# Performance work log

Measured on AMD Instinct MI355X. Metric: run time of the kernel, lower is better.

The kernel has to match this reference:

```python
import jax, jax.numpy as jnp
import numpy as np
import math

D_MODEL = 1024
N_HEADS = 16
D_K = D_MODEL // N_HEADS
MAX_REL = 128


def setup_inputs() -> dict:
    key = jax.random.key(0)
    ks = jax.random.split(key, 10)
    B, S = 2, 2048
    std = 1.0 / math.sqrt(D_MODEL)
    inp = {
        "x": jax.random.normal(ks[0], (B, S, D_MODEL), dtype=jnp.float32),
        "Wq": jax.random.normal(ks[1], (D_MODEL, D_MODEL), dtype=jnp.float32) * std,
        "bq": jnp.zeros((D_MODEL,), dtype=jnp.float32),
        "Wk": jax.random.normal(ks[2], (D_MODEL, D_MODEL), dtype=jnp.float32) * std,
        "bk": jnp.zeros((D_MODEL,), dtype=jnp.float32),
        "Wv": jax.random.normal(ks[3], (D_MODEL, D_MODEL), dtype=jnp.float32) * std,
        "bv": jnp.zeros((D_MODEL,), dtype=jnp.float32),
        "Wo": jax.random.normal(ks[4], (D_MODEL, D_MODEL), dtype=jnp.float32) * std,
        "bo": jnp.zeros((D_MODEL,), dtype=jnp.float32),
        "rel_bias": jax.random.normal(ks[5], (N_HEADS, 2 * MAX_REL + 1), dtype=jnp.float32) * 0.02,
    }
    return inp


def _rel_bias_matrix(rel_bias, seq_len):
    # (H, S, S) gathered relative-position bias
    pos = jnp.arange(seq_len)
    rel = pos[:, None] - pos[None, :]
    idx = jnp.clip(rel, -MAX_REL, MAX_REL) + MAX_REL  # (S, S) in [0, 2M]
    return rel_bias[:, idx]  # (H, S, S)


def reference(x, Wq, bq, Wk, bk, Wv, bv, Wo, bo, rel_bias):
    B, S, _ = x.shape
    def proj(W, b):
        y = x @ W.T + b  # torch Linear: x @ W^T + b
        return y.reshape(B, S, N_HEADS, D_K).transpose(0, 2, 1, 3)  # (B,H,S,Dk)
    Q, K, V = proj(Wq, bq), proj(Wk, bk), proj(Wv, bv)
    scores = jnp.einsum("bhqd,bhkd->bhqk", Q, K) / math.sqrt(D_K)
    scores = scores + _rel_bias_matrix(rel_bias, S)[None]
    attn = jax.nn.softmax(scores, axis=-1)
    out = jnp.einsum("bhqk,bhkd->bhqd", attn, V)
    out = out.transpose(0, 2, 1, 3).reshape(B, S, D_MODEL)
    return out @ Wo.T + bo
```

## Files before the change

### kernel.cpp

```cpp
#include <hip/hip_runtime.h>

static constexpr int DM = 1024;
static constexpr int NH = 16;
static constexpr int DK = 64;
static constexpr int S  = 2048;
static constexpr int B  = 2;
static constexpr float LOG2E = 1.4426950408889634f;
static constexpr float FMAX  = 11.0f;
static constexpr int NSPLIT = 4;

typedef _Float16 f16;
typedef _Float16 f16x8 __attribute__((ext_vector_type(8)));
typedef _Float16 f16x4 __attribute__((ext_vector_type(4)));
typedef float    f32x4 __attribute__((ext_vector_type(4)));

static constexpr size_t NX = (size_t)B * S * DM;
static constexpr size_t NW = (size_t)DM * DM;

__global__ __launch_bounds__(256) void cvt_f16(const float* __restrict__ x,
                                               const float* __restrict__ wq,
                                               const float* __restrict__ wk,
                                               const float* __restrict__ wv,
                                               const float* __restrict__ wo,
                                               f16* __restrict__ xh,
                                               f16* __restrict__ wqh,
                                               f16* __restrict__ wkh,
                                               f16* __restrict__ wvh,
                                               f16* __restrict__ woh)
{
    const size_t base = ((size_t)blockIdx.x * 256 + threadIdx.x) * 8;
    const float* src; f16* dst; size_t off;
    if (base < NX) { src = x; dst = xh; off = base; }
    else {
        const size_t rem = base - NX;
        const int seg = (int)(rem >> 20);
        off = rem & (NW - 1);
        src = seg == 0 ? wq : (seg == 1 ? wk : (seg == 2 ? wv : wo));
        dst = seg == 0 ? wqh : (seg == 1 ? wkh : (seg == 2 ? wvh : woh));
    }
    float4 a = *(const float4*)&src[off];
    float4 b = *(const float4*)&src[off + 4];
    f16x8 h = { (f16)a.x, (f16)a.y, (f16)a.z, (f16)a.w,
                (f16)b.x, (f16)b.y, (f16)b.z, (f16)b.w };
    *(f16x8*)&dst[off] = h;
}

template<int MODE>
__global__ __launch_bounds__(256) void gemm_h(const f16* __restrict__ A,
                                              const f16* __restrict__ W0,
                                              const f16* __restrict__ W1,
                                              const f16* __restrict__ W2,
                                              const float* __restrict__ b0,
                                              const float* __restrict__ b1,
                                              const float* __restrict__ b2,
                                              void* __restrict__ o0,
                                              void* __restrict__ o1,
                                              void* __restrict__ o2)
{
    __shared__ f16 As[128 * 72];
    __shared__ f16 Bs[128 * 72];

    const int t    = threadIdx.x;
    const int w    = t >> 6;
    const int lane = t & 63;
    const int tx   = lane & 15;
    const int quad = lane >> 4;
    const int wm   = w >> 1;
    const int wn   = w & 1;
    const int m0   = blockIdx.y * 128;

    const f16* W; const float* bias; f16* outh = nullptr; float* outf = nullptr;
    float scale; int n0;
    if (MODE == 0) {
        const int wsel = blockIdx.x >> 3;
        n0   = (blockIdx.x & 7) * 128;
        W    = wsel == 0 ? W0 : (wsel == 1 ? W1 : W2);
        bias = wsel == 0 ? b0 : (wsel == 1 ? b1 : b2);
        outh = (f16*)(wsel == 0 ? o0 : (wsel == 1 ? o1 : o2));
        scale = wsel == 0 ? LOG2E * 0.125f : 1.0f;
    } else {
        n0 = blockIdx.x * 128;
        W = W0; bias = b0; outf = (float*)o0; scale = 1.0f;
    }

    const int lr = t >> 2;
    const int lc = (t & 3) * 8;

    f32x4 acc[4][4];
#pragma unroll
    for (int mt = 0; mt < 4; ++mt)
#pragma unroll
        for (int nt = 0; nt < 4; ++nt) acc[mt][nt] = (f32x4){0.f, 0.f, 0.f, 0.f};

    f16x8 ga[4], gb[4];
    {
        const f16* Ap = A + (size_t)(m0 + lr) * DM + lc;
        const f16* Wp = W + (size_t)(n0 + lr) * DM + lc;
        ga[0] = *(const f16x8*)(Ap);
        ga[1] = *(const f16x8*)(Ap + 32);
        ga[2] = *(const f16x8*)(Ap + (size_t)64 * DM);
        ga[3] = *(const f16x8*)(Ap + (size_t)64 * DM + 32);
        gb[0] = *(const f16x8*)(Wp);
        gb[1] = *(const f16x8*)(Wp + 32);
        gb[2] = *(const f16x8*)(Wp + (size_t)64 * DM);
        gb[3] = *(const f16x8*)(Wp + (size_t)64 * DM + 32);
    }

    for (int k0 = 0; k0 < DM; k0 += 64) {
        __syncthreads();
        *(f16x8*)&As[ lr       * 72 + lc     ] = ga[0];
        *(f16x8*)&As[ lr       * 72 + lc + 32] = ga[1];
        *(f16x8*)&As[(lr + 64) * 72 + lc     ] = ga[2];
        *(f16x8*)&As[(lr + 64) * 72 + lc + 32] = ga[3];
        *(f16x8*)&Bs[ lr       * 72 + lc     ] = gb[0];
        *(f16x8*)&Bs[ lr       * 72 + lc + 32] = gb[1];
        *(f16x8*)&Bs[(lr + 64) * 72 + lc     ] = gb[2];
        *(f16x8*)&Bs[(lr + 64) * 72 + lc + 32] = gb[3];
        if (k0 + 64 < DM) {
            const f16* Ap = A + (size_t)(m0 + lr) * DM + k0 + 64 + lc;
            const f16* Wp = W + (size_t)(n0 + lr) * DM + k0 + 64 + lc;
            ga[0] = *(const f16x8*)(Ap);
            ga[1] = *(const f16x8*)(Ap + 32);
            ga[2] = *(const f16x8*)(Ap + (size_t)64 * DM);
            ga[3] = *(const f16x8*)(Ap + (size_t)64 * DM + 32);
            gb[0] = *(const f16x8*)(Wp);
            gb[1] = *(const f16x8*)(Wp + 32);
            gb[2] = *(const f16x8*)(Wp + (size_t)64 * DM);
            gb[3] = *(const f16x8*)(Wp + (size_t)64 * DM + 32);
        }
        __syncthreads();

        f16x8 af[4][2];
#pragma unroll
        for (int mt = 0; mt < 4; ++mt)
#pragma unroll
            for (int ks = 0; ks < 2; ++ks)
                af[mt][ks] = *(const f16x8*)&As[(wm*64 + mt*16 + tx)*72 + ks*32 + quad*8];
#pragma unroll
        for (int nt = 0; nt < 4; ++nt) {
#pragma unroll
            for (int ks = 0; ks < 2; ++ks) {
                f16x8 bf = *(const f16x8*)&Bs[(wn*64 + nt*16 + tx)*72 + ks*32 + quad*8];
#pragma unroll
                for (int mt = 0; mt < 4; ++mt)
                    acc[mt][nt] = __builtin_amdgcn_mfma_f32_16x16x32_f16(af[mt][ks], bf, acc[mt][nt], 0, 0, 0);
            }
        }
    }

#pragma unroll
    for (int nt = 0; nt < 4; ++nt) {
        const int n = n0 + wn*64 + nt*16 + tx;
        const float bn = bias[n];
#pragma unroll
        for (int mt = 0; mt < 4; ++mt)
#pragma unroll
            for (int r = 0; r < 4; ++r) {
                const int m = m0 + wm*64 + mt*16 + quad*4 + r;
                const float v = (acc[mt][nt][r] + bn) * scale;
                if (MODE == 0) {
                    const int bi = m >> 11;
                    const int ss = m & (S - 1);
                    const int h  = n >> 6;
                    const int dk = n & (DK - 1);
                    outh[((size_t)((bi*NH + h)*S + ss))*DK + dk] = (f16)v;
                } else {
                    outf[(size_t)m * DM + n] = v;
                }
            }
    }
}

__global__ __launch_bounds__(256, 4) void attn_v4(const f16* __restrict__ Q,
                                                  const f16* __restrict__ K,
                                                  const f16* __restrict__ V,
                                                  const float* __restrict__ relb,
                                                  f16* __restrict__ On,
                                                  float* __restrict__ lp)
{
    __shared__ f16 Ks[64*72];
    __shared__ f16 Vt[64*72];
    __shared__ float rb2[257];

    const int t    = threadIdx.x;
    const int w    = t >> 6;
    const int lane = t & 63;
    const int tx   = lane & 15;
    const int quad = lane >> 4;
    const int qt   = blockIdx.x >> 2;
    const int sp   = blockIdx.x & 3;
    const int h    = blockIdx.y;
    const int b    = blockIdx.z;
    const int q0   = qt * 128;

    const f16* Qb = Q + (size_t)((b*NH + h) * S) * DK;
    const f16* Kb = K + (size_t)((b*NH + h) * S) * DK;
    const f16* Vb = V + (size_t)((b*NH + h) * S) * DK;

    for (int i = t; i < 257; i += 256) rb2[i] = relb[h*257 + i] * LOG2E - FMAX;

    const int qrow = q0 + w*32 + tx;
    f16x8 qf[2][2];
#pragma unroll
    for (int qb = 0; qb < 2; ++qb)
#pragma unroll
        for (int ks = 0; ks < 2; ++ks)
            qf[qb][ks] = *(const f16x8*)(Qb + (size_t)(qrow + qb*16)*DK + ks*32 + quad*8);

    f32x4 oT[4][2];
    float lsum[2] = {0.f, 0.f};
#pragma unroll
    for (int d = 0; d < 4; ++d)
#pragma unroll
        for (int qb = 0; qb < 2; ++qb) oT[d][qb] = (f32x4){0.f, 0.f, 0.f, 0.f};

    const int kt0 = sp * (S / 64 / NSPLIT);
    for (int kt = kt0; kt < kt0 + S/64/NSPLIT; ++kt) {
        const int k0 = kt * 64;

        const int seq = t & 63, d0k = (t >> 6) * 16;
        f16x8 kr0 = *(const f16x8*)(Kb + (size_t)(k0 + seq)*DK + d0k);
        f16x8 kr1 = *(const f16x8*)(Kb + (size_t)(k0 + seq)*DK + d0k + 8);
        const int s2 = (t & 31) * 2, d0v = (t >> 5) * 8;
        f16x8 vr0 = *(const f16x8*)(Vb + (size_t)(k0 + s2    )*DK + d0v);
        f16x8 vr1 = *(const f16x8*)(Vb + (size_t)(k0 + s2 + 1)*DK + d0v);

        __syncthreads();
        *(f16x8*)&Ks[seq*72 + d0k    ] = kr0;
        *(f16x8*)&Ks[seq*72 + d0k + 8] = kr1;
        {
            const int g = ((s2 >> 2) & 3)*16 + (s2 >> 4)*4 + (s2 & 3);
            const unsigned short* u0 = (const unsigned short*)&vr0;
            const unsigned short* u1 = (const unsigned short*)&vr1;
#pragma unroll
            for (int j = 0; j < 8; ++j) {
                unsigned int pw = (unsigned int)u0[j] | ((unsigned int)u1[j] << 16);
                *(unsigned int*)&Vt[(d0v + j)*72 + g] = pw;
            }
        }
        __syncthreads();

        const bool farlo = (k0 - q0) >= 256;
        const bool farhi = (q0 - k0) >= 192;
        const float bconst = farlo ? rb2[0] : rb2[256];
        const int relbase = (q0 + w*32 + tx) - (k0 + quad*4);

        f16x4 pf[4][2];
#pragma unroll
        for (int sb = 0; sb < 4; ++sb) {
            f32x4 sT[2];
            if (farlo | farhi) {
                sT[0] = (f32x4){bconst, bconst, bconst, bconst};
                sT[1] = sT[0];
            } else {
#pragma unroll
                for (int qb = 0; qb < 2; ++qb)
#pragma unroll
                    for (int r = 0; r < 4; ++r) {
                        int rel = relbase + qb*16 - sb*16 - r;
                        rel = rel < -128 ? -128 : (rel > 128 ? 128 : rel);
                        sT[qb][r] = rb2[rel + 128];
                    }
            }
#pragma unroll
            for (int ks = 0; ks < 2; ++ks) {
                f16x8 kf = *(const f16x8*)&Ks[(sb*16 + tx)*72 + ks*32 + quad*8];
#pragma unroll
                for (int qb = 0; qb < 2; ++qb)
                    sT[qb] = __builtin_amdgcn_mfma_f32_16x16x32_f16(kf, qf[qb][ks], sT[qb], 0, 0, 0);
            }
#pragma unroll
            for (int qb = 0; qb < 2; ++qb)
#pragma unroll
                for (int r = 0; r < 4; ++r) {
                    const float p = exp2f(sT[qb][r]);
                    lsum[qb] += p;
                    pf[sb][qb][r] = (f16)p;
                }
        }

#pragma unroll
        for (int d = 0; d < 4; ++d) {
#pragma unroll
            for (int sp2 = 0; sp2 < 2; ++sp2) {
                f16x8 vv = *(const f16x8*)&Vt[(d*16 + tx)*72 + quad*16 + sp2*8];
                f16x4 vlo = __builtin_shufflevector(vv, vv, 0, 1, 2, 3);
                f16x4 vhi = __builtin_shufflevector(vv, vv, 4, 5, 6, 7);
#pragma unroll
                for (int qb = 0; qb < 2; ++qb) {
                    oT[d][qb] = __builtin_amdgcn_mfma_f32_16x16x16f16(vlo, pf[sp2*2    ][qb], oT[d][qb], 0, 0, 0);
                    oT[d][qb] = __builtin_amdgcn_mfma_f32_16x16x16f16(vhi, pf[sp2*2 + 1][qb], oT[d][qb], 0, 0, 0);
                }
            }
        }
    }

#pragma unroll
    for (int qb = 0; qb < 2; ++qb) {
        float l = lsum[qb];
        l += __shfl_xor(l, 16);
        l += __shfl_xor(l, 32);
        const int q = q0 + w*32 + qb*16 + tx;
        if (quad == 0)
            lp[(((size_t)sp*B + b)*NH + h)*S + q] = l;
#pragma unroll
        for (int d = 0; d < 4; ++d) {
            f16x4 hv = { (f16)oT[d][qb][0], (f16)oT[d][qb][1],
                         (f16)oT[d][qb][2], (f16)oT[d][qb][3] };
            *(f16x4*)&On[(size_t)sp*NX + ((size_t)(b*S + q))*DM + h*DK + d*16 + quad*4] = hv;
        }
    }
}

__global__ __launch_bounds__(256) void combine(const f16* __restrict__ On,
                                               const float* __restrict__ lp,
                                               f16* __restrict__ AOh)
{
    const size_t i8 = ((size_t)blockIdx.x * 256 + threadIdx.x) * 8;
    const int token = (int)(i8 >> 10);
    const int c     = (int)(i8 & (DM - 1));
    const int b     = token >> 11;
    const int st    = token & (S - 1);
    const int h     = c >> 6;
    float l = 0.f;
#pragma unroll
    for (int sp = 0; sp < NSPLIT; ++sp)
        l += lp[(((size_t)sp*B + b)*NH + h)*S + st];
    const float inv = 1.0f / l;
    float acc[8];
#pragma unroll
    for (int j = 0; j < 8; ++j) acc[j] = 0.f;
#pragma unroll
    for (int sp = 0; sp < NSPLIT; ++sp) {
        f16x8 v = *(const f16x8*)&On[(size_t)sp*NX + i8];
#pragma unroll
        for (int j = 0; j < 8; ++j) acc[j] += (float)v[j];
    }
    f16x8 o;
#pragma unroll
    for (int j = 0; j < 8; ++j) o[j] = (f16)(acc[j] * inv);
    *(f16x8*)&AOh[i8] = o;
}

extern "C" void kernel_launch(void* const* d_in, const int* in_sizes, int n_in,
                              void* d_out, int out_size, void* d_ws, size_t ws_size,
                              hipStream_t stream)
{
    const float* x    = (const float*)d_in[0];
    const float* Wq   = (const float*)d_in[1];
    const float* bq   = (const float*)d_in[2];
    const float* Wk   = (const float*)d_in[3];
    const float* bk   = (const float*)d_in[4];
    const float* Wv   = (const float*)d_in[5];
    const float* bv   = (const float*)d_in[6];
    const float* Wo   = (const float*)d_in[7];
    const float* bo   = (const float*)d_in[8];
    const float* relb = (const float*)d_in[9];

    f16* Xh  = (f16*)d_ws;
    f16* Wqh = Xh  + NX;
    f16* Wkh = Wqh + NW;
    f16* Wvh = Wkh + NW;
    f16* Woh = Wvh + NW;
    f16* Qh  = Woh + NW;
    f16* Kh  = Qh  + NX;
    f16* Vh  = Kh  + NX;
    f16* AOh = Vh  + NX;
    f16* On  = AOh + NX;
    float* lpart = (float*)(On + (size_t)NSPLIT*NX);

    cvt_f16<<<(NX + 4*NW) / (256*8), 256, 0, stream>>>(x, Wq, Wk, Wv, Wo,
                                                       Xh, Wqh, Wkh, Wvh, Woh);
    gemm_h<0><<<dim3(24, 32), 256, 0, stream>>>(Xh, Wqh, Wkh, Wvh,
                                                bq, bk, bv, Qh, Kh, Vh);
    attn_v4<<<dim3((S/128)*NSPLIT, NH, B), 256, 0, stream>>>(Qh, Kh, Vh, relb, On, lpart);
    combine<<<NX / (256*8), 256, 0, stream>>>(On, lpart, AOh);
    gemm_h<1><<<dim3(8, 32), 256, 0, stream>>>(AOh, Woh, nullptr, nullptr,
                                               bo, nullptr, nullptr,
                                               d_out, nullptr, nullptr);
}
```

Measured before the change: 221.2 us.

## Drop split-K attention and combine kernel; double-buffer K/V tiles with register prefetch

Removes the four-way key split and the separate combine kernel, so each block walks all 32 key tiles and normalises its output directly. K/V tiles are double-buffered in shared memory, with the next tile prefetched into registers while the current one is computed, which needs only one barrier per iteration. Softmax probabilities are packed with cvt_pkrtz. This cuts the partial-output traffic and a kernel launch, but the grid shrinks to 512 blocks, so there is less parallelism and each block runs a longer serial loop.

```diff
diff --git a/kernel.cpp b/kernel.cpp
--- a/kernel.cpp
+++ b/kernel.cpp
@@ -7,11 +7,11 @@
 static constexpr int B  = 2;
 static constexpr float LOG2E = 1.4426950408889634f;
 static constexpr float FMAX  = 11.0f;
-static constexpr int NSPLIT = 4;
 
 typedef _Float16 f16;
 typedef _Float16 f16x8 __attribute__((ext_vector_type(8)));
 typedef _Float16 f16x4 __attribute__((ext_vector_type(4)));
+typedef __fp16   h16x2 __attribute__((ext_vector_type(2)));
 typedef float    f32x4 __attribute__((ext_vector_type(4)));
 
 static constexpr size_t NX = (size_t)B * S * DM;
@@ -171,15 +171,14 @@
     }
 }
 
-__global__ __launch_bounds__(256, 4) void attn_v4(const f16* __restrict__ Q,
+__global__ __launch_bounds__(256, 4) void attn_v5(const f16* __restrict__ Q,
                                                   const f16* __restrict__ K,
                                                   const f16* __restrict__ V,
                                                   const float* __restrict__ relb,
-                                                  f16* __restrict__ On,
-                                                  float* __restrict__ lp)
+                                                  f16* __restrict__ aout)
 {
-    __shared__ f16 Ks[64*72];
-    __shared__ f16 Vt[64*72];
+    __shared__ f16 Ks[2 * 64*72];
+    __shared__ f16 Vt[2 * 64*72];
     __shared__ float rb2[257];
 
     const int t    = threadIdx.x;
@@ -187,11 +186,9 @@
     const int lane = t & 63;
     const int tx   = lane & 15;
     const int quad = lane >> 4;
-    const int qt   = blockIdx.x >> 2;
-    const int sp   = blockIdx.x & 3;
+    const int q0   = blockIdx.x * 128;
     const int h    = blockIdx.y;
     const int b    = blockIdx.z;
-    const int q0   = qt * 128;
 
     const f16* Qb = Q + (size_t)((b*NH + h) * S) * DK;
     const f16* Kb = K + (size_t)((b*NH + h) * S) * DK;
@@ -214,31 +211,41 @@
 #pragma unroll
         for (int qb = 0; qb < 2; ++qb) oT[d][qb] = (f32x4){0.f, 0.f, 0.f, 0.f};
 
-    const int kt0 = sp * (S / 64 / NSPLIT);
-    for (int kt = kt0; kt < kt0 + S/64/NSPLIT; ++kt) {
+    const int seq = t & 63, d0k = (t >> 6) * 16;
+    const int s2 = (t & 31) * 2, d0v = (t >> 5) * 8;
+    const int g = ((s2 >> 2) & 3)*16 + (s2 >> 4)*4 + (s2 & 3);
+
+    f16x8 kr0 = *(const f16x8*)(Kb + (size_t)seq*DK + d0k);
+    f16x8 kr1 = *(const f16x8*)(Kb + (size_t)seq*DK + d0k + 8);
+    f16x8 vr0 = *(const f16x8*)(Vb + (size_t)s2*DK + d0v);
+    f16x8 vr1 = *(const f16x8*)(Vb + (size_t)(s2 + 1)*DK + d0v);
+
+    for (int kt = 0; kt < S/64; ++kt) {
         const int k0 = kt * 64;
-
-        const int seq = t & 63, d0k = (t >> 6) * 16;
-        f16x8 kr0 = *(const f16x8*)(Kb + (size_t)(k0 + seq)*DK + d0k);
-        f16x8 kr1 = *(const f16x8*)(Kb + (size_t)(k0 + seq)*DK + d0k + 8);
-        const int s2 = (t & 31) * 2, d0v = (t >> 5) * 8;
-        f16x8 vr0 = *(const f16x8*)(Vb + (size_t)(k0 + s2    )*DK + d0v);
-        f16x8 vr1 = *(const f16x8*)(Vb + (size_t)(k0 + s2 + 1)*DK + d0v);
-
-        __syncthreads();
-        *(f16x8*)&Ks[seq*72 + d0k    ] = kr0;
-        *(f16x8*)&Ks[seq*72 + d0k + 8] = kr1;
+        const int db = (kt & 1) * 4608;
+        f16* KsW = &Ks[db];
+        f16* VtW = &Vt[db];
+
+        *(f16x8*)&KsW[seq*72 + d0k    ] = kr0;
+        *(f16x8*)&KsW[seq*72 + d0k + 8] = kr1;
         {
-            const int g = ((s2 >> 2) & 3)*16 + (s2 >> 4)*4 + (s2 & 3);
             const unsigned short* u0 = (const unsigned short*)&vr0;
             const unsigned short* u1 = (const unsigned short*)&vr1;
 #pragma unroll
             for (int j = 0; j < 8; ++j) {
                 unsigned int pw = (unsigned int)u0[j] | ((unsigned int)u1[j] << 16);
-                *(unsigned int*)&Vt[(d0v + j)*72 + g] = pw;
+                *(unsigned int*)&VtW[(d0v + j)*72 + g] = pw;
             }
         }
         __syncthreads();
+
+        if (kt + 1 < S/64) {
+            const int k0n = k0 + 64;
+            kr0 = *(const f16x8*)(Kb + (size_t)(k0n + seq)*DK + d0k);
+            kr1 = *(const f16x8*)(Kb + (size_t)(k0n + seq)*DK + d0k + 8);
+            vr0 = *(const f16x8*)(Vb + (size_t)(k0n + s2    )*DK + d0v);
+            vr1 = *(const f16x8*)(Vb + (size_t)(k0n + s2 + 1)*DK + d0v);
+        }
 
         const bool farlo = (k0 - q0) >= 256;
         const bool farhi = (q0 - k0) >= 192;
@@ -264,26 +271,29 @@
             }
 #pragma unroll
             for (int ks = 0; ks < 2; ++ks) {
-                f16x8 kf = *(const f16x8*)&Ks[(sb*16 + tx)*72 + ks*32 + quad*8];
+                f16x8 kf = *(const f16x8*)&KsW[(sb*16 + tx)*72 + ks*32 + quad*8];
 #pragma unroll
                 for (int qb = 0; qb < 2; ++qb)
                     sT[qb] = __builtin_amdgcn_mfma_f32_16x16x32_f16(kf, qf[qb][ks], sT[qb], 0, 0, 0);
             }
 #pragma unroll
-            for (int qb = 0; qb < 2; ++qb)
-#pragma unroll
-                for (int r = 0; r < 4; ++r) {
-                    const float p = exp2f(sT[qb][r]);
-                    lsum[qb] += p;
-                    pf[sb][qb][r] = (f16)p;
-                }
+            for (int qb = 0; qb < 2; ++qb) {
+                const float p0 = exp2f(sT[qb][0]);
+                const float p1 = exp2f(sT[qb][1]);
+                const float p2 = exp2f(sT[qb][2]);
+                const float p3 = exp2f(sT[qb][3]);
+                lsum[qb] += (p0 + p1) + (p2 + p3);
+                h16x2 lo = __builtin_amdgcn_cvt_pkrtz(p0, p1);
+                h16x2 hi = __builtin_amdgcn_cvt_pkrtz(p2, p3);
+                pf[sb][qb] = (f16x4){ (f16)lo.x, (f16)lo.y, (f16)hi.x, (f16)hi.y };
+            }
         }
 
 #pragma unroll
         for (int d = 0; d < 4; ++d) {
 #pragma unroll
             for (int sp2 = 0; sp2 < 2; ++sp2) {
-                f16x8 vv = *(const f16x8*)&Vt[(d*16 + tx)*72 + quad*16 + sp2*8];
+                f16x8 vv = *(const f16x8*)&VtW[(d*16 + tx)*72 + quad*16 + sp2*8];
                 f16x4 vlo = __builtin_shufflevector(vv, vv, 0, 1, 2, 3);
                 f16x4 vhi = __builtin_shufflevector(vv, vv, 4, 5, 6, 7);
 #pragma unroll
@@ -300,46 +310,16 @@
         float l = lsum[qb];
         l += __shfl_xor(l, 16);
         l += __shfl_xor(l, 32);
+        const float inv = 1.0f / l;
         const int q = q0 + w*32 + qb*16 + tx;
-        if (quad == 0)
-            lp[(((size_t)sp*B + b)*NH + h)*S + q] = l;
 #pragma unroll
         for (int d = 0; d < 4; ++d) {
-            f16x4 hv = { (f16)oT[d][qb][0], (f16)oT[d][qb][1],
-                         (f16)oT[d][qb][2], (f16)oT[d][qb][3] };
-            *(f16x4*)&On[(size_t)sp*NX + ((size_t)(b*S + q))*DM + h*DK + d*16 + quad*4] = hv;
-        }
-    }
-}
-
-__global__ __launch_bounds__(256) void combine(const f16* __restrict__ On,
-                                               const float* __restrict__ lp,
-                                               f16* __restrict__ AOh)
-{
-    const size_t i8 = ((size_t)blockIdx.x * 256 + threadIdx.x) * 8;
-    const int token = (int)(i8 >> 10);
-    const int c     = (int)(i8 & (DM - 1));
-    const int b     = token >> 11;
-    const int st    = token & (S - 1);
-    const int h     = c >> 6;
-    float l = 0.f;
-#pragma unroll
-    for (int sp = 0; sp < NSPLIT; ++sp)
-        l += lp[(((size_t)sp*B + b)*NH + h)*S + st];
-    const float inv = 1.0f / l;
-    float acc[8];
-#pragma unroll
-    for (int j = 0; j < 8; ++j) acc[j] = 0.f;
-#pragma unroll
-    for (int sp = 0; sp < NSPLIT; ++sp) {
-        f16x8 v = *(const f16x8*)&On[(size_t)sp*NX + i8];
-#pragma unroll
-        for (int j = 0; j < 8; ++j) acc[j] += (float)v[j];
-    }
-    f16x8 o;
-#pragma unroll
-    for (int j = 0; j < 8; ++j) o[j] = (f16)(acc[j] * inv);
-    *(f16x8*)&AOh[i8] = o;
+            h16x2 e0 = __builtin_amdgcn_cvt_pkrtz(oT[d][qb][0]*inv, oT[d][qb][1]*inv);
+            h16x2 e1 = __builtin_amdgcn_cvt_pkrtz(oT[d][qb][2]*inv, oT[d][qb][3]*inv);
+            f16x4 hv = { (f16)e0.x, (f16)e0.y, (f16)e1.x, (f16)e1.y };
+            *(f16x4*)&aout[((size_t)(b*S + q))*DM + h*DK + d*16 + quad*4] = hv;
+        }
+    }
 }
 
 extern "C" void kernel_launch(void* const* d_in, const int* in_sizes, int n_in,
@@ -366,15 +346,12 @@
     f16* Kh  = Qh  + NX;
     f16* Vh  = Kh  + NX;
     f16* AOh = Vh  + NX;
-    f16* On  = AOh + NX;
-    float* lpart = (float*)(On + (size_t)NSPLIT*NX);
 
     cvt_f16<<<(NX + 4*NW) / (256*8), 256, 0, stream>>>(x, Wq, Wk, Wv, Wo,
                                                        Xh, Wqh, Wkh, Wvh, Woh);
     gemm_h<0><<<dim3(24, 32), 256, 0, stream>>>(Xh, Wqh, Wkh, Wvh,
                                                 bq, bk, bv, Qh, Kh, Vh);
-    attn_v4<<<dim3((S/128)*NSPLIT, NH, B), 256, 0, stream>>>(Qh, Kh, Vh, relb, On, lpart);
-    combine<<<NX / (256*8), 256, 0, stream>>>(On, lpart, AOh);
+    attn_v5<<<dim3(S/128, NH, B), 256, 0, stream>>>(Qh, Kh, Vh, relb, AOh);
     gemm_h<1><<<dim3(8, 32), 256, 0, stream>>>(AOh, Woh, nullptr, nullptr,
                                                bo, nullptr, nullptr,
                                                d_out, nullptr, nullptr);
```

Measured after the change: 235.4 us. 6.4% more time.
